# Performance work log

Measured on AMD Instinct MI355X. Metric: run time of the kernel, lower is better.

## Reference

```python
import jax, jax.numpy as jnp
import numpy as np

KSIZE = 7      # gaussian kernel size (SecondMomentMatrixLayer default)
SIGMA = 5.0    # gaussian sigma (default)
ALPHA = 0.05   # corner response alpha (CornerResponseLayer default)


def _gaussian_kernel(ksize, sigma):
    ax = np.arange(ksize, dtype=np.float64) - ksize // 2
    g1 = np.exp(-(ax ** 2) / (2.0 * sigma ** 2))
    k2 = np.outer(g1, g1)
    return (k2 / k2.sum()).astype(np.float32)


def setup_inputs() -> dict:
    key = jax.random.key(0)
    x = jax.random.normal(key, (4, 1, 2048, 2048), dtype=jnp.float32)
    # Sobel filters (ImageGradientsLayer): out-channels [Ix, Iy], shape (2,1,3,3)
    sobel_kernel = jnp.array(
        [[[[-1.0, 0.0, 1.0], [-2.0, 0.0, 2.0], [-1.0, 0.0, 1.0]]],
         [[[-1.0, -2.0, -1.0], [0.0, 0.0, 0.0], [1.0, 2.0, 1.0]]]],
        dtype=jnp.float32)
    # Depthwise (groups=3) gaussian kernel, shape (3,1,7,7)
    g = jnp.asarray(_gaussian_kernel(KSIZE, SIGMA))
    gauss_kernel = jnp.tile(g[None, None], (3, 1, 1, 1))
    return {"x": x, "sobel_kernel": sobel_kernel, "gauss_kernel": gauss_kernel}


def _conv(x, k, pad, groups=1):
    # torch Conv2d is cross-correlation; so is lax.conv_general_dilated
    return jax.lax.conv_general_dilated(
        x, k, window_strides=(1, 1), padding=[(pad, pad), (pad, pad)],
        dimension_numbers=("NCHW", "OIHW", "NCHW"), feature_group_count=groups)


def reference(x, sobel_kernel, gauss_kernel):
    # 1) image gradients via Sobel: (N,1,H,W) -> (N,2,H,W)
    grads = _conv(x, sobel_kernel, pad=1)
    Ix, Iy = grads[:, 0], grads[:, 1]
    # 2) channel products: I_xx, I_yy, I_xy -> (N,3,H,W)
    prods = jnp.stack([Ix * Ix, Iy * Iy, Ix * Iy], axis=1)
    # 3) gaussian-weighted second moments (depthwise conv, groups=3)
    S = _conv(prods, gauss_kernel, pad=KSIZE // 2, groups=3)
    Sxx, Syy, Sxy = S[:, 0], S[:, 1], S[:, 2]
    # 4) corner response R = det - alpha * trace^2 -> (N,1,H,W)
    trace = Sxx + Syy
    R = (Sxx * Syy - Sxy * Sxy - ALPHA * trace * trace)[:, None]
    # 5) NMS: global-median threshold, 7x7 stride-1 maxpool, binarize, scale by R
    median = jnp.quantile(R, 0.5, method="lower")  # torch.median = lower median
    thr = jnp.where(R < median, jnp.float32(0.0), R)
    pooled = jax.lax.reduce_window(
        thr, -jnp.inf, jax.lax.max, window_dimensions=(1, 1, 7, 7),
        window_strides=(1, 1, 1, 1),
        padding=[(0, 0), (0, 0), (3, 3), (3, 3)])
    binarized = jnp.where(thr == pooled, jnp.float32(1.0), jnp.float32(0.0))
    return binarized * R
```

## Files before the change

### kernel.cpp

```cpp
#include <hip/hip_runtime.h>
#include <math.h>

constexpr int IMH = 2048, IMW = 2048, NB = 4;
constexpr int NPIX = NB * IMH * IMW;
constexpr unsigned KSEL = 8388607u;

__device__ __forceinline__ unsigned f2u(float f) {
    unsigned b = __float_as_uint(f);
    return (b & 0x80000000u) ? ~b : (b | 0x80000000u);
}

__device__ __forceinline__ void gauss7(float* a) {
    const double g0 = 0.8352702114112720;
    const double g1 = 0.9231163463866358;
    const double g2 = 0.9801986733067553;
    const double s = 2.0 * (g0 + g1 + g2) + 1.0;
    const double inv = 1.0 / s;
    a[0] = a[6] = (float)(g0 * inv);
    a[1] = a[5] = (float)(g1 * inv);
    a[2] = a[4] = (float)(g2 * inv);
    a[3] = (float)inv;
}

__device__ __forceinline__ float2 fmax2(float2 a, float2 b) {
    return make_float2(fmaxf(a.x, b.x), fmaxf(a.y, b.y));
}

template<bool CHK>
__device__ __forceinline__ void hblur_fused(const float* SX, float* STH, const float* a,
                                            int r, int g, int x0, int y0) {
    const float* p0 = SX + r * 72 + 4 * g;
    const float* p1 = p0 + 72;
    const float* p2 = p1 + 72;
    float4 A0 = *(const float4*)(p0), B0 = *(const float4*)(p0 + 4), C0 = *(const float4*)(p0 + 8);
    float4 A1 = *(const float4*)(p1), B1 = *(const float4*)(p1 + 4), C1 = *(const float4*)(p1 + 8);
    float4 A2 = *(const float4*)(p2), B2 = *(const float4*)(p2 + 4), C2 = *(const float4*)(p2 + 8);
    float w0[12] = {A0.x, A0.y, A0.z, A0.w, B0.x, B0.y, B0.z, B0.w, C0.x, C0.y, C0.z, C0.w};
    float w1[12] = {A1.x, A1.y, A1.z, A1.w, B1.x, B1.y, B1.z, B1.w, C1.x, C1.y, C1.z, C1.w};
    float w2[12] = {A2.x, A2.y, A2.z, A2.w, B2.x, B2.y, B2.z, B2.w, C2.x, C2.y, C2.z, C2.w};

    float cS[12];
    #pragma unroll
    for (int j = 0; j < 12; ++j) cS[j] = w0[j] + 2.0f * w1[j] + w2[j];
    float ix[10], iy[10];
    #pragma unroll
    for (int j = 0; j < 10; ++j) {
        ix[j] = cS[j + 2] - cS[j];
        float rS2 = w2[j] + 2.0f * w2[j + 1] + w2[j + 2];
        float rS0 = w0[j] + 2.0f * w0[j + 1] + w0[j + 2];
        iy[j] = rS2 - rS0;
        if (CHK) {
            int gy = y0 - 3 + r, gx = x0 - 3 + (4 * g + j);
            if (!((unsigned)gy < (unsigned)IMH && (unsigned)gx < (unsigned)IMW)) {
                ix[j] = 0.f; iy[j] = 0.f;
            }
        }
    }
    float sxx[4], syy[4], sxy[4];
    #pragma unroll
    for (int k = 0; k < 4; ++k) {
        float xx = 0.f, yy = 0.f, xy = 0.f;
        #pragma unroll
        for (int d = 0; d < 7; ++d) {
            float vx = ix[k + d], vy = iy[k + d];
            float t = a[d] * vx;
            xx += t * vx;
            xy += t * vy;
            yy += (a[d] * vy) * vy;
        }
        sxx[k] = xx; syy[k] = yy; sxy[k] = xy;
    }
    *(float4*)&STH[r * 64 + 4 * g]        = make_float4(sxx[0], sxx[1], sxx[2], sxx[3]);
    *(float4*)&STH[2432 + r * 64 + 4 * g] = make_float4(syy[0], syy[1], syy[2], syy[3]);
    *(float4*)&STH[4864 + r * 64 + 4 * g] = make_float4(sxy[0], sxy[1], sxy[2], sxy[3]);
}

__launch_bounds__(256, 4)
__global__ void harris_R(const float* __restrict__ x, float* __restrict__ Rout,
                         unsigned* __restrict__ hist) {
    __shared__ __align__(16) float smem[10176];
    float* STH = smem;
    float* SX = smem + 7296;
    unsigned* LH = (unsigned*)(smem + 7296);

    const int tid = threadIdx.x;
    const int tx = tid & 63, ty = tid >> 6;
    const int x0 = blockIdx.x * 64, y0 = blockIdx.y * 32, b = blockIdx.z;
    const float* xb = x + (size_t)b * IMH * IMW;
    const bool interior = (x0 >= 4) && (x0 + 68 <= IMW) && (y0 >= 4) && (y0 + 36 <= IMH);

    if (interior) {
        const float* xp = xb + (size_t)(y0 - 4) * IMW + (x0 - 4);
        #pragma unroll
        for (int k = 0; k < 3; ++k) {
            int i = tid + k * 256;
            if (i < 720) {
                int r = i / 18, c4 = i - r * 18;
                *(float4*)&SX[r * 72 + 4 * c4] = *(const float4*)&xp[(size_t)r * IMW + 4 * c4];
            }
        }
    } else {
        for (int i = tid; i < 2880; i += 256) {
            int r = i / 72, c = i - r * 72;
            int gy = y0 - 4 + r, gx = x0 - 4 + c;
            float v = 0.f;
            if ((unsigned)gy < (unsigned)IMH && (unsigned)gx < (unsigned)IMW)
                v = xb[(size_t)gy * IMW + gx];
            SX[r * 72 + c] = v;
        }
    }
    __syncthreads();

    float a[7]; gauss7(a);

    if (interior) {
        #pragma unroll
        for (int k = 0; k < 3; ++k) {
            int i = tid + k * 256;
            if (i < 608) { int r = i >> 4, g = i & 15; hblur_fused<false>(SX, STH, a, r, g, x0, y0); }
        }
    } else {
        #pragma unroll
        for (int k = 0; k < 3; ++k) {
            int i = tid + k * 256;
            if (i < 608) { int r = i >> 4, g = i & 15; hblur_fused<true>(SX, STH, a, r, g, x0, y0); }
        }
    }
    __syncthreads();

    for (int i = tid; i < 2048; i += 256) LH[i] = 0u;

    float vxx[14], vyy[14], vxy[14];
    {
        const float* base = STH + (8 * ty) * 64 + tx;
        #pragma unroll
        for (int t = 0; t < 14; ++t) {
            vxx[t] = base[t * 64];
            vyy[t] = base[2432 + t * 64];
            vxy[t] = base[4864 + t * 64];
        }
    }
    float rv[8];
    float* Rb = Rout + (size_t)b * IMH * IMW + (size_t)y0 * IMW + x0;
    #pragma unroll
    for (int j = 0; j < 8; ++j) {
        float sxx = 0.f, syy = 0.f, sxy = 0.f;
        #pragma unroll
        for (int d = 0; d < 7; ++d) {
            sxx += a[d] * vxx[j + d];
            syy += a[d] * vyy[j + d];
            sxy += a[d] * vxy[j + d];
        }
        float tr = sxx + syy;
        float R = sxx * syy - sxy * sxy - 0.05f * tr * tr;
        rv[j] = R;
        Rb[(size_t)(8 * ty + j) * IMW + tx] = R;
    }
    __syncthreads();

    #pragma unroll
    for (int j = 0; j < 8; ++j) atomicAdd(&LH[f2u(rv[j]) >> 21], 1u);
    __syncthreads();

    const unsigned slot = ((blockIdx.z * gridDim.y + blockIdx.y) * gridDim.x + blockIdx.x) & 7u;
    for (int i = tid; i < 2048; i += 256) {
        unsigned c = LH[i];
        if (c) atomicAdd(&hist[i * 8 + slot], c);
    }
}

__global__ void zero_kernel(unsigned* __restrict__ p, int n, int kidx, unsigned kval) {
    int i = blockIdx.x * blockDim.x + threadIdx.x;
    if (i < n) p[i] = (i == kidx) ? kval : 0u;
}

__global__ void hist2_kernel(const float* __restrict__ R, unsigned* __restrict__ hist,
                             const unsigned* __restrict__ sel) {
    __shared__ unsigned lh[4096];
    for (int i = threadIdx.x; i < 4096; i += 256) lh[i] = 0u;
    __syncthreads();
    const unsigned pref = sel[1];
    const float4* R4 = (const float4*)R;
    const int n4 = NPIX / 4;
    for (int i = (blockIdx.x * 256 + threadIdx.x) * 2; i < n4; i += gridDim.x * 512) {
        float4 v0 = R4[i];
        float4 v1 = R4[i + 1];
        unsigned u;
        u = f2u(v0.x); if ((u >> 21) == pref) atomicAdd(&lh[(u >> 9) & 0xFFFu], 1u);
        u = f2u(v0.y); if ((u >> 21) == pref) atomicAdd(&lh[(u >> 9) & 0xFFFu], 1u);
        u = f2u(v0.z); if ((u >> 21) == pref) atomicAdd(&lh[(u >> 9) & 0xFFFu], 1u);
        u = f2u(v0.w); if ((u >> 21) == pref) atomicAdd(&lh[(u >> 9) & 0xFFFu], 1u);
        u = f2u(v1.x); if ((u >> 21) == pref) atomicAdd(&lh[(u >> 9) & 0xFFFu], 1u);
        u = f2u(v1.y); if ((u >> 21) == pref) atomicAdd(&lh[(u >> 9) & 0xFFFu], 1u);
        u = f2u(v1.z); if ((u >> 21) == pref) atomicAdd(&lh[(u >> 9) & 0xFFFu], 1u);
        u = f2u(v1.w); if ((u >> 21) == pref) atomicAdd(&lh[(u >> 9) & 0xFFFu], 1u);
    }
    __syncthreads();
    for (int i = threadIdx.x; i < 4096; i += 256) { unsigned c = lh[i]; if (c) atomicAdd(&hist[i], c); }
}

__global__ void hist3_kernel(const float* __restrict__ R, unsigned* __restrict__ hist,
                             const unsigned* __restrict__ sel) {
    __shared__ unsigned lh[512];
    if (threadIdx.x < 256) { lh[threadIdx.x] = 0u; lh[threadIdx.x + 256] = 0u; }
    __syncthreads();
    const unsigned pref = sel[1];
    const float4* R4 = (const float4*)R;
    const int n4 = NPIX / 4;
    for (int i = (blockIdx.x * 256 + threadIdx.x) * 2; i < n4; i += gridDim.x * 512) {
        float4 v0 = R4[i];
        float4 v1 = R4[i + 1];
        unsigned u;
        u = f2u(v0.x); if ((u >> 9) == pref) atomicAdd(&lh[u & 0x1FFu], 1u);
        u = f2u(v0.y); if ((u >> 9) == pref) atomicAdd(&lh[u & 0x1FFu], 1u);
        u = f2u(v0.z); if ((u >> 9) == pref) atomicAdd(&lh[u & 0x1FFu], 1u);
        u = f2u(v0.w); if ((u >> 9) == pref) atomicAdd(&lh[u & 0x1FFu], 1u);
        u = f2u(v1.x); if ((u >> 9) == pref) atomicAdd(&lh[u & 0x1FFu], 1u);
        u = f2u(v1.y); if ((u >> 9) == pref) atomicAdd(&lh[u & 0x1FFu], 1u);
        u = f2u(v1.z); if ((u >> 9) == pref) atomicAdd(&lh[u & 0x1FFu], 1u);
        u = f2u(v1.w); if ((u >> 9) == pref) atomicAdd(&lh[u & 0x1FFu], 1u);
    }
    __syncthreads();
    if (threadIdx.x < 256) {
        unsigned c = lh[threadIdx.x]; if (c) atomicAdd(&hist[threadIdx.x], c);
        c = lh[threadIdx.x + 256]; if (c) atomicAdd(&hist[threadIdx.x + 256], c);
    }
}

__global__ void select_kernel(const unsigned* __restrict__ hist, unsigned* __restrict__ sel,
                              int bpt, int bits, int final_stage, int slots) {
    __shared__ unsigned part[256];
    __shared__ unsigned grp[16];
    __shared__ int chs;
    __shared__ unsigned runs;
    const int t = threadIdx.x;
    const unsigned krem = sel[0];
    unsigned s = 0;
    for (int i = 0; i < bpt; ++i) {
        unsigned bsum = 0;
        for (int j = 0; j < slots; ++j) bsum += hist[(t * bpt + i) * slots + j];
        s += bsum;
    }
    part[t] = s;
    __syncthreads();
    #pragma unroll
    for (int off = 1; off < 256; off <<= 1) {
        unsigned add = (t >= off) ? part[t - off] : 0u;
        __syncthreads();
        part[t] += add;
        __syncthreads();
    }
    unsigned incl = part[t];
    unsigned excl = incl - s;
    if (excl <= krem && krem < incl) { chs = t; runs = excl; }
    __syncthreads();
    int ch = chs;
    if (t < bpt) {
        unsigned g = 0;
        for (int j = 0; j < slots; ++j) g += hist[(ch * bpt + t) * slots + j];
        grp[t] = g;
    }
    __syncthreads();
    if (t == 0) {
        unsigned r2 = runs; int bsel = ch * bpt;
        for (int j = 0; j < bpt; ++j) {
            unsigned h = grp[j];
            if (r2 + h > krem) { bsel = ch * bpt + j; break; }
            r2 += h;
        }
        sel[0] = krem - r2;
        unsigned pref = (sel[1] << bits) | (unsigned)bsel;
        sel[1] = pref;
        if (final_stage) {
            unsigned fb = (pref & 0x80000000u) ? (pref ^ 0x80000000u) : ~pref;
            ((float*)sel)[2] = __uint_as_float(fb);
        }
    }
}

__launch_bounds__(512, 6)
__global__ void harris_out(const float* __restrict__ R, const unsigned* __restrict__ sel,
                           float* __restrict__ out) {
    __shared__ __align__(16) float smem2[9520];
    float* SR = smem2;
    float2* SM2 = (float2*)(smem2 + 5040);
    const float med = ((const float*)sel)[2];
    const int tid = threadIdx.x;
    const int x0 = blockIdx.x * 64, y0 = blockIdx.y * 64, b = blockIdx.z;
    const float* Rb = R + (size_t)b * IMH * IMW;

    for (int i = tid; i < 70 * 70; i += 512) {
        int r = i / 70, c = i - r * 70;
        int gy = y0 - 3 + r, gx = x0 - 3 + c;
        float v = -INFINITY;
        if ((unsigned)gy < (unsigned)IMH && (unsigned)gx < (unsigned)IMW)
            v = Rb[(size_t)gy * IMW + gx];
        SR[r * 72 + c] = v;
    }
    __syncthreads();

    for (int i = tid; i < 70 * 32; i += 512) {
        int r = i >> 5, p = i & 31;
        const float2* u = (const float2*)(SR + r * 72 + 2 * p);
        float2 u0 = u[0], u1 = u[1], u2 = u[2], u3 = u[3];
        float cv[8] = {u0.x, u0.y, u1.x, u1.y, u2.x, u2.y, u3.x, u3.y};
        float tv[8];
        #pragma unroll
        for (int k = 0; k < 8; ++k) {
            float v = cv[k];
            tv[k] = (v < med) ? ((v == -INFINITY) ? -INFINITY : 0.0f) : v;
        }
        float mid = fmaxf(fmaxf(fmaxf(tv[1], tv[2]), fmaxf(tv[3], tv[4])), fmaxf(tv[5], tv[6]));
        SM2[r * 32 + p] = make_float2(fmaxf(tv[0], mid), fmaxf(tv[7], mid));
    }
    __syncthreads();

    const int p = tid & 31, g = tid >> 5;
    float2 vm[10];
    #pragma unroll
    for (int t = 0; t < 10; ++t) vm[t] = SM2[(4 * g + t) * 32 + p];
    float2 m2[9];
    #pragma unroll
    for (int i = 0; i < 9; ++i) m2[i] = fmax2(vm[i], vm[i + 1]);
    float2 m4[7];
    #pragma unroll
    for (int i = 0; i < 7; ++i) m4[i] = fmax2(m2[i], m2[i + 2]);
    float* ob = out + (size_t)b * IMH * IMW + (size_t)y0 * IMW + x0;
    #pragma unroll
    for (int j = 0; j < 4; ++j) {
        float2 pooled = fmax2(m4[j], m4[j + 3]);
        float vA = SR[(4 * g + j + 3) * 72 + 2 * p + 3];
        float vB = SR[(4 * g + j + 3) * 72 + 2 * p + 4];
        float tA = (vA < med) ? 0.0f : vA;
        float tB = (vB < med) ? 0.0f : vB;
        float2 o = make_float2((tA == pooled.x) ? vA : 0.0f, (tB == pooled.y) ? vB : 0.0f);
        *(float2*)&ob[(size_t)(4 * g + j) * IMW + 2 * p] = o;
    }
}

extern "C" void kernel_launch(void* const* d_in, const int* in_sizes, int n_in,
                              void* d_out, int out_size, void* d_ws, size_t ws_size,
                              hipStream_t stream) {
    const float* x = (const float*)d_in[0];
    float* out = (float*)d_out;

    const size_t needed = (size_t)NPIX * 4 + (16384 + 4096 + 512 + 8) * 4;
    if (ws_size < needed) return;
    float* R = (float*)d_ws;
    unsigned* hbase = (unsigned*)((char*)d_ws + (size_t)NPIX * 4);
    unsigned* h1 = hbase;
    unsigned* h2 = hbase + 16384;
    unsigned* h3 = hbase + 20480;
    unsigned* sel = hbase + 20992;

    zero_kernel<<<(21000 + 255) / 256, 256, 0, stream>>>(hbase, 21000, 20992, KSEL);

    dim3 rgrid(IMW / 64, IMH / 32, NB);
    harris_R<<<rgrid, 256, 0, stream>>>(x, R, h1);

    select_kernel<<<1, 256, 0, stream>>>(h1, sel, 8, 11, 0, 8);
    hist2_kernel<<<2048, 256, 0, stream>>>(R, h2, sel);
    select_kernel<<<1, 256, 0, stream>>>(h2, sel, 16, 12, 0, 1);
    hist3_kernel<<<2048, 256, 0, stream>>>(R, h3, sel);
    select_kernel<<<1, 256, 0, stream>>>(h3, sel, 2, 9, 1, 1);

    dim3 ogrid(IMW / 64, IMH / 64, NB);
    harris_out<<<ogrid, 512, 0, stream>>>(R, sel, out);
}
```

Baseline: 311.5 us.

## Split fused Harris R kernel into separable horizontal and vertical passes via workspace

Replaces the single tiled harris_R kernel with two kernels. The first computes Sobel gradients and the horizontal Gaussian blur of the three products, writing them to a workspace buffer. The second does the vertical blur, corner response and histogram. The split is processed in row bands sized to fit the available workspace, and the original kernel remains as a fallback. It aims to remove shared-memory halo overhead and recomputation, but adds a full global-memory round trip for three intermediate planes.

```diff
diff --git a/kernel.cpp b/kernel.cpp
--- a/kernel.cpp
+++ b/kernel.cpp
@@ -24,6 +24,134 @@
 
 __device__ __forceinline__ float2 fmax2(float2 a, float2 b) {
     return make_float2(fmaxf(a.x, b.x), fmaxf(a.y, b.y));
+}
+
+
+__global__ void passA(const float* __restrict__ x, float* __restrict__ STH,
+                      int sr0, int nsr, size_t ps) {
+    const int tid = threadIdx.x;
+    const int G = blockIdx.x * 16 + (tid & 15);
+    const int srow = blockIdx.y * 16 + (tid >> 4);
+    if (srow >= nsr) return;
+    const int b = blockIdx.z;
+    const int r = sr0 + srow;
+    float* out0 = STH + ((size_t)b * 3 + 0) * ps + (size_t)srow * IMW + 4 * G;
+    float* out1 = STH + ((size_t)b * 3 + 1) * ps + (size_t)srow * IMW + 4 * G;
+    float* out2 = STH + ((size_t)b * 3 + 2) * ps + (size_t)srow * IMW + 4 * G;
+    if ((unsigned)r >= (unsigned)IMH) {
+        *(float4*)out0 = make_float4(0.f, 0.f, 0.f, 0.f);
+        *(float4*)out1 = make_float4(0.f, 0.f, 0.f, 0.f);
+        *(float4*)out2 = make_float4(0.f, 0.f, 0.f, 0.f);
+        return;
+    }
+    const float* xb = x + (size_t)b * IMH * IMW;
+    const int cb = 4 * G - 4;
+    float w0[12], w1[12], w2[12];
+    const bool fast = (cb >= 0) && (cb + 12 <= IMW) && (r >= 1) && (r <= IMH - 2);
+    if (fast) {
+        const float* p0 = xb + (size_t)(r - 1) * IMW + cb;
+        const float* p1 = p0 + IMW;
+        const float* p2 = p1 + IMW;
+        float4 A0 = *(const float4*)(p0), B0 = *(const float4*)(p0 + 4), C0 = *(const float4*)(p0 + 8);
+        float4 A1 = *(const float4*)(p1), B1 = *(const float4*)(p1 + 4), C1 = *(const float4*)(p1 + 8);
+        float4 A2 = *(const float4*)(p2), B2 = *(const float4*)(p2 + 4), C2 = *(const float4*)(p2 + 8);
+        w0[0]=A0.x; w0[1]=A0.y; w0[2]=A0.z; w0[3]=A0.w; w0[4]=B0.x; w0[5]=B0.y; w0[6]=B0.z; w0[7]=B0.w; w0[8]=C0.x; w0[9]=C0.y; w0[10]=C0.z; w0[11]=C0.w;
+        w1[0]=A1.x; w1[1]=A1.y; w1[2]=A1.z; w1[3]=A1.w; w1[4]=B1.x; w1[5]=B1.y; w1[6]=B1.z; w1[7]=B1.w; w1[8]=C1.x; w1[9]=C1.y; w1[10]=C1.z; w1[11]=C1.w;
+        w2[0]=A2.x; w2[1]=A2.y; w2[2]=A2.z; w2[3]=A2.w; w2[4]=B2.x; w2[5]=B2.y; w2[6]=B2.z; w2[7]=B2.w; w2[8]=C2.x; w2[9]=C2.y; w2[10]=C2.z; w2[11]=C2.w;
+    } else {
+        #pragma unroll
+        for (int j = 0; j < 12; ++j) {
+            int gx = cb + j;
+            bool cok = (unsigned)gx < (unsigned)IMW;
+            w0[j] = (cok && r - 1 >= 0) ? xb[(size_t)(r - 1) * IMW + gx] : 0.f;
+            w1[j] = cok ? xb[(size_t)r * IMW + gx] : 0.f;
+            w2[j] = (cok && r + 1 < IMH) ? xb[(size_t)(r + 1) * IMW + gx] : 0.f;
+        }
+    }
+    float cS[12];
+    #pragma unroll
+    for (int j = 0; j < 12; ++j) cS[j] = w0[j] + 2.0f * w1[j] + w2[j];
+    float ix[10], iy[10];
+    #pragma unroll
+    for (int j = 0; j < 10; ++j) {
+        ix[j] = cS[j + 2] - cS[j];
+        float rS2 = w2[j] + 2.0f * w2[j + 1] + w2[j + 2];
+        float rS0 = w0[j] + 2.0f * w0[j + 1] + w0[j + 2];
+        iy[j] = rS2 - rS0;
+    }
+    if (G == 0 || G == 511) {
+        #pragma unroll
+        for (int j = 0; j < 10; ++j) {
+            int gx = cb + 1 + j;
+            if (!((unsigned)gx < (unsigned)IMW)) { ix[j] = 0.f; iy[j] = 0.f; }
+        }
+    }
+    float a[7]; gauss7(a);
+    float sxx[4], syy[4], sxy[4];
+    #pragma unroll
+    for (int k = 0; k < 4; ++k) {
+        float xx = 0.f, yy = 0.f, xy = 0.f;
+        #pragma unroll
+        for (int d = 0; d < 7; ++d) {
+            float vx = ix[k + d], vy = iy[k + d];
+            float t = a[d] * vx;
+            xx += t * vx;
+            xy += t * vy;
+            yy += (a[d] * vy) * vy;
+        }
+        sxx[k] = xx; syy[k] = yy; sxy[k] = xy;
+    }
+    *(float4*)out0 = make_float4(sxx[0], sxx[1], sxx[2], sxx[3]);
+    *(float4*)out1 = make_float4(syy[0], syy[1], syy[2], syy[3]);
+    *(float4*)out2 = make_float4(sxy[0], sxy[1], sxy[2], sxy[3]);
+}
+
+__global__ void passB(const float* __restrict__ STH, float* __restrict__ Rout,
+                      unsigned* __restrict__ hist, int band_start, size_t ps) {
+    __shared__ unsigned LH[2048];
+    const int tid = threadIdx.x;
+    for (int i = tid; i < 2048; i += 256) LH[i] = 0u;
+    const int p = blockIdx.x * 256 + tid;
+    const int r0 = band_start + blockIdx.y * 8;
+    const int b = blockIdx.z;
+    const int srbase = blockIdx.y * 8;
+    const float* pl0 = STH + ((size_t)b * 3 + 0) * ps + (size_t)srbase * IMW + 2 * p;
+    const float* pl1 = STH + ((size_t)b * 3 + 1) * ps + (size_t)srbase * IMW + 2 * p;
+    const float* pl2 = STH + ((size_t)b * 3 + 2) * ps + (size_t)srbase * IMW + 2 * p;
+    float2 vxx[14], vyy[14], vxy[14];
+    #pragma unroll
+    for (int t = 0; t < 14; ++t) {
+        vxx[t] = *(const float2*)&pl0[(size_t)t * IMW];
+        vyy[t] = *(const float2*)&pl1[(size_t)t * IMW];
+        vxy[t] = *(const float2*)&pl2[(size_t)t * IMW];
+    }
+    float a[7]; gauss7(a);
+    __syncthreads();
+    float* Rb = Rout + (size_t)b * IMH * IMW + (size_t)r0 * IMW + 2 * p;
+    #pragma unroll
+    for (int j = 0; j < 8; ++j) {
+        float sxxA = 0.f, syyA = 0.f, sxyA = 0.f;
+        float sxxB = 0.f, syyB = 0.f, sxyB = 0.f;
+        #pragma unroll
+        for (int d = 0; d < 7; ++d) {
+            sxxA += a[d] * vxx[j + d].x;  sxxB += a[d] * vxx[j + d].y;
+            syyA += a[d] * vyy[j + d].x;  syyB += a[d] * vyy[j + d].y;
+            sxyA += a[d] * vxy[j + d].x;  sxyB += a[d] * vxy[j + d].y;
+        }
+        float trA = sxxA + syyA;
+        float RA = sxxA * syyA - sxyA * sxyA - 0.05f * trA * trA;
+        float trB = sxxB + syyB;
+        float RB = sxxB * syyB - sxyB * sxyB - 0.05f * trB * trB;
+        *(float2*)&Rb[(size_t)j * IMW] = make_float2(RA, RB);
+        atomicAdd(&LH[f2u(RA) >> 21], 1u);
+        atomicAdd(&LH[f2u(RB) >> 21], 1u);
+    }
+    __syncthreads();
+    const unsigned slot = ((blockIdx.z * gridDim.y + blockIdx.y) * gridDim.x + blockIdx.x) & 7u;
+    for (int i = tid; i < 2048; i += 256) {
+        unsigned c = LH[i];
+        if (c) atomicAdd(&hist[i * 8 + slot], c);
+    }
 }
 
 template<bool CHK>
@@ -38,7 +166,6 @@
     float w0[12] = {A0.x, A0.y, A0.z, A0.w, B0.x, B0.y, B0.z, B0.w, C0.x, C0.y, C0.z, C0.w};
     float w1[12] = {A1.x, A1.y, A1.z, A1.w, B1.x, B1.y, B1.z, B1.w, C1.x, C1.y, C1.z, C1.w};
     float w2[12] = {A2.x, A2.y, A2.z, A2.w, B2.x, B2.y, B2.z, B2.w, C2.x, C2.y, C2.z, C2.w};
-
     float cS[12];
     #pragma unroll
     for (int j = 0; j < 12; ++j) cS[j] = w0[j] + 2.0f * w1[j] + w2[j];
@@ -344,19 +471,39 @@
     const float* x = (const float*)d_in[0];
     float* out = (float*)d_out;
 
-    const size_t needed = (size_t)NPIX * 4 + (16384 + 4096 + 512 + 8) * 4;
-    if (ws_size < needed) return;
+    const size_t base_need = (size_t)NPIX * 4 + (16384 + 4096 + 512 + 8) * 4;
+    if (ws_size < base_need) return;
     float* R = (float*)d_ws;
     unsigned* hbase = (unsigned*)((char*)d_ws + (size_t)NPIX * 4);
     unsigned* h1 = hbase;
     unsigned* h2 = hbase + 16384;
     unsigned* h3 = hbase + 20480;
     unsigned* sel = hbase + 20992;
+    float* STH = (float*)((char*)d_ws + ((base_need + 255) & ~(size_t)255));
+
+    int nbands = 0;
+    for (int cand = 1; cand <= 4; cand <<= 1) {
+        size_t sth_bytes = 12ull * ((IMH / cand) + 6) * IMW * 4;
+        if (ws_size >= ((base_need + 255) & ~(size_t)255) + sth_bytes) { nbands = cand; break; }
+    }
 
     zero_kernel<<<(21000 + 255) / 256, 256, 0, stream>>>(hbase, 21000, 20992, KSEL);
 
-    dim3 rgrid(IMW / 64, IMH / 32, NB);
-    harris_R<<<rgrid, 256, 0, stream>>>(x, R, h1);
+    if (nbands) {
+        const int band_rows = IMH / nbands;
+        const size_t ps = (size_t)(band_rows + 6) * IMW;
+        for (int band = 0; band < nbands; ++band) {
+            const int bs = band * band_rows;
+            const int sr0 = bs - 3, nsr = band_rows + 6;
+            dim3 ga(IMW / 64, (nsr + 15) / 16, NB);
+            passA<<<ga, 256, 0, stream>>>(x, STH, sr0, nsr, ps);
+            dim3 gb(IMW / 512, band_rows / 8, NB);
+            passB<<<gb, 256, 0, stream>>>(STH, R, h1, bs, ps);
+        }
+    } else {
+        dim3 rgrid(IMW / 64, IMH / 32, NB);
+        harris_R<<<rgrid, 256, 0, stream>>>(x, R, h1);
+    }
 
     select_kernel<<<1, 256, 0, stream>>>(h1, sel, 8, 11, 0, 8);
     hist2_kernel<<<2048, 256, 0, stream>>>(R, h2, sel);
```

Result: no change. 316.2 us (+1.5%).
